# Kernel optimization log

Hardware: AMD Instinct MI355X
Metric: run time of the kernel (lower is better)

Reference implementation:

```python
import jax, jax.numpy as jnp
import numpy as np

SIGMA = 1.0  # init kwarg sigma

def _rbf_kernel(A):
    # K[i,j] = exp(-0.5 * ||a_i - a_j||^2 / sigma^2)
    sq = jnp.sum(A * A, axis=1)                      # [n]
    d2 = sq[:, None] + sq[None, :] - 2.0 * (A @ A.T)  # [n, n]
    return jnp.exp(-0.5 * d2 / (SIGMA ** 2))

def _double_center(K):
    # C K C with C = I - 11^T/n, done in O(n^2) via mean subtraction
    row = K.mean(axis=1, keepdims=True)
    col = K.mean(axis=0, keepdims=True)
    tot = K.mean()
    return K - row - col + tot

def setup_inputs() -> dict:
    key = jax.random.key(0)
    kx, ky = jax.random.split(key)
    X = jax.random.normal(kx, (4096, 512), dtype=jnp.float32)
    Y = jax.random.normal(ky, (4096, 512), dtype=jnp.float32)
    return {"X": X, "Y": Y}

def reference(X, Y):
    n = X.shape[0]
    KXc = _double_center(_rbf_kernel(X))
    KYc = _double_center(_rbf_kernel(Y))
    # trace(KX C KY C) = sum(center(KX) * center(KY)) since K symmetric, C idempotent
    hsic = jnp.sum(KXc * KYc) / ((n - 1) ** 2)
    return hsic
```

## Files before the change

### kernel.cpp

```cpp
#include <hip/hip_runtime.h>
#include <hip/hip_bf16.h>

namespace {

constexpr int N = 4096;
constexpr int D = 512;
constexpr int BM = 128;
constexpr int BK = 64;
constexpr int KITERS = D / BK;
constexpr int NB = N / BM;
constexpr int NBLK = NB * (NB + 1) / 2;
constexpr int TILEB = BM * BK;
constexpr int PANELB = BM * D;

constexpr size_t OFF_XB  = 0;
constexpr size_t OFF_YB  = (size_t)N * D;
constexpr size_t OFF_SQX = OFF_YB + (size_t)N * D;
constexpr size_t OFF_SQY = OFF_SQX + (size_t)N * 4;
constexpr size_t OFF_SX  = OFF_SQY + (size_t)N * 4;
constexpr size_t OFF_SY  = OFF_SX + (size_t)N * 4;
constexpr size_t OFF_T1  = OFF_SY + (size_t)N * 4;
constexpr size_t WS_NEED = OFF_T1 + 4;


constexpr float D2_SKIP = 240.f;

typedef __attribute__((ext_vector_type(4))) float floatx4;
typedef __attribute__((ext_vector_type(2))) long longx2;

__device__ inline void stage16(const void* g, void* l) {
  __builtin_amdgcn_global_load_lds(
      (const __attribute__((address_space(1))) unsigned int*)g,
      (__attribute__((address_space(3))) unsigned int*)l, 16, 0, 0);
}

__global__ void prep_kernel(const float* __restrict__ X, const float* __restrict__ Y,
                            unsigned char* __restrict__ Xf8, unsigned char* __restrict__ Yf8,
                            float* __restrict__ sqX, float* __restrict__ sqY,
                            float* __restrict__ sX, float* __restrict__ sY,
                            float* __restrict__ T1) {
  const int wave = threadIdx.x >> 6, lane = threadIdx.x & 63;
  const int row = blockIdx.x * 4 + wave;
  const int m = blockIdx.y;
  const float* __restrict__ src = m ? Y : X;
  unsigned char* __restrict__ dst = m ? Yf8 : Xf8;
  float* __restrict__ dsq = m ? sqY : sqX;

  if (threadIdx.x < 4) {
    float* z = m ? sY : sX;
    z[blockIdx.x * 4 + threadIdx.x] = 0.f;
  }
  if (blockIdx.x == 0 && m == 0 && threadIdx.x == 0) *T1 = 0.f;

  const float4* s4 = (const float4*)(src + (size_t)row * D);
  float4 v0 = s4[lane * 2];
  float4 v1 = s4[lane * 2 + 1];
  float acc = v0.x * v0.x + v0.y * v0.y + v0.z * v0.z + v0.w * v0.w
            + v1.x * v1.x + v1.y * v1.y + v1.z * v1.z + v1.w * v1.w;

  unsigned int w0 = 0, w1 = 0;
  w0 = __builtin_amdgcn_cvt_pk_fp8_f32(v0.x, v0.y, w0, false);
  w0 = __builtin_amdgcn_cvt_pk_fp8_f32(v0.z, v0.w, w0, true);
  w1 = __builtin_amdgcn_cvt_pk_fp8_f32(v1.x, v1.y, w1, false);
  w1 = __builtin_amdgcn_cvt_pk_fp8_f32(v1.z, v1.w, w1, true);
  const unsigned long long pk =
      (unsigned long long)w0 | ((unsigned long long)w1 << 32);

  const int p    = row >> 7;
  const int half = (row >> 6) & 1;
  const int nib  = (row >> 4) & 3;
  const int cl   = row & 15;
  const int ks   = lane >> 3;
  const int pass = (lane >> 2) & 1;
  const int quad = lane & 3;
  const size_t off = (size_t)p * PANELB + (size_t)ks * TILEB +
                     half * 4096 + nib * 1024 + quad * 256 + cl * 16 + pass * 8;
  *(unsigned long long*)(dst + off) = pk;

#pragma unroll
  for (int mm = 32; mm >= 1; mm >>= 1) acc += __shfl_xor(acc, mm, 64);
  if (lane == 0) dsq[row] = acc;
}

__launch_bounds__(256, 2)
__global__ void hsic_main(const unsigned char* __restrict__ Xf8,
                          const unsigned char* __restrict__ Yf8,
                          const float* __restrict__ sqX, const float* __restrict__ sqY,
                          float* __restrict__ sX, float* __restrict__ sY,
                          float* __restrict__ T1) {
  __shared__ __align__(16) unsigned char smem[2][4 * TILEB];

  const int b = blockIdx.x;
  int idx = (b & 7) * (NBLK / 8) + (b >> 3);

  const float nf = (float)NB + 0.5f;
  int bI = (int)(nf - sqrtf(nf * nf - 2.0f * (float)idx));
  if (bI < 0) bI = 0;
  if (bI >= NB) bI = NB - 1;
  while (bI * NB - bI * (bI - 1) / 2 > idx) --bI;
  while ((bI + 1) * NB - (bI + 1) * bI / 2 <= idx) ++bI;
  const int bJ = bI + (idx - (bI * NB - bI * (bI - 1) / 2));
  const bool offdiag = (bI != bJ);

  const int tid = threadIdx.x;
  const int lane = tid & 63, wave = tid >> 6;
  const int wm = wave >> 1, wn = wave & 1;
  const int quad = lane >> 4, cl = lane & 15;

  const unsigned char* gAx = Xf8 + (size_t)bI * PANELB;
  const unsigned char* gBx = Xf8 + (size_t)bJ * PANELB;
  const unsigned char* gAy = Yf8 + (size_t)bI * PANELB;
  const unsigned char* gBy = Yf8 + (size_t)bJ * PANELB;

  floatx4 accX[4][4];
  floatx4 accY[4][4];
#pragma unroll
  for (int i = 0; i < 4; ++i)
#pragma unroll
    for (int j = 0; j < 4; ++j) {
      accX[i][j] = (floatx4){0.f, 0.f, 0.f, 0.f};
      accY[i][j] = (floatx4){0.f, 0.f, 0.f, 0.f};
    }

  auto stage_all = [&](int kt, int buf) {
    const size_t ks0 = (size_t)kt * TILEB;
#pragma unroll
    for (int h = 0; h < 2; ++h) {
      const int c = tid + h * 256;
      const size_t goff = ks0 + (size_t)c * 16;
      const int loff = c * 16;
      stage16(gAx + goff, &smem[buf][0 * TILEB + loff]);
      stage16(gBx + goff, &smem[buf][1 * TILEB + loff]);
      stage16(gAy + goff, &smem[buf][2 * TILEB + loff]);
      stage16(gBy + goff, &smem[buf][3 * TILEB + loff]);
    }
  };

  stage_all(0, 0);

  for (int kt = 0; kt < KITERS; ++kt) {
    const int buf = kt & 1;
    __syncthreads();
    if (kt + 1 < KITERS) stage_all(kt + 1, buf ^ 1);

    const unsigned char* Ax = &smem[buf][0 * TILEB];
    const unsigned char* Bx = &smem[buf][1 * TILEB];
    const unsigned char* Ay = &smem[buf][2 * TILEB];
    const unsigned char* By = &smem[buf][3 * TILEB];

    longx2 bxf[4], byf[4];
#pragma unroll
    for (int ni = 0; ni < 4; ++ni) {
      const int off = wn * 4096 + ni * 1024 + (lane << 4);
      bxf[ni] = *(const longx2*)&Bx[off];
      byf[ni] = *(const longx2*)&By[off];
    }
#pragma unroll
    for (int mi = 0; mi < 4; ++mi) {
      const int off = wm * 4096 + mi * 1024 + (lane << 4);
      const longx2 axf = *(const longx2*)&Ax[off];
      const longx2 ayf = *(const longx2*)&Ay[off];
#pragma unroll
      for (int ni = 0; ni < 4; ++ni) {
        accX[mi][ni] = __builtin_amdgcn_mfma_f32_16x16x32_fp8_fp8(axf[0], bxf[ni][0], accX[mi][ni], 0, 0, 0);
        accX[mi][ni] = __builtin_amdgcn_mfma_f32_16x16x32_fp8_fp8(axf[1], bxf[ni][1], accX[mi][ni], 0, 0, 0);
        accY[mi][ni] = __builtin_amdgcn_mfma_f32_16x16x32_fp8_fp8(ayf[0], byf[ni][0], accY[mi][ni], 0, 0, 0);
        accY[mi][ni] = __builtin_amdgcn_mfma_f32_16x16x32_fp8_fp8(ayf[1], byf[ni][1], accY[mi][ni], 0, 0, 0);
      }
    }
  }

  const int Ib = bI * BM + wm * 64;
  const int Jb = bJ * BM + wn * 64;
  float t1l = 0.f;
  float rx[4][4], ry[4][4];
  float cx[4], cy[4];
#pragma unroll
  for (int mi = 0; mi < 4; ++mi)
#pragma unroll
    for (int r = 0; r < 4; ++r) { rx[mi][r] = 0.f; ry[mi][r] = 0.f; }
#pragma unroll
  for (int ni = 0; ni < 4; ++ni) { cx[ni] = 0.f; cy[ni] = 0.f; }

  bool wave_any = false;

#pragma unroll
  for (int mi = 0; mi < 4; ++mi) {
    const int ig0 = Ib + mi * 16 + quad * 4;
    float sxi[4], syi[4];
#pragma unroll
    for (int r = 0; r < 4; ++r) { sxi[r] = sqX[ig0 + r]; syi[r] = sqY[ig0 + r]; }
#pragma unroll
    for (int ni = 0; ni < 4; ++ni) {
      const int jg = Jb + ni * 16 + cl;
      const float sxj = sqX[jg];
      const float syj = sqY[jg];
      float d2x[4], d2y[4];
      bool lflag = false;
#pragma unroll
      for (int r = 0; r < 4; ++r) {
        const int ig = ig0 + r;
        d2x[r] = sxi[r] + sxj - 2.f * accX[mi][ni][r];
        d2y[r] = syi[r] + syj - 2.f * accY[mi][ni][r];
        lflag |= (d2x[r] < D2_SKIP) | (d2y[r] < D2_SKIP) | (ig == jg);
      }
      if (__any(lflag)) {
        wave_any = true;
#pragma unroll
        for (int r = 0; r < 4; ++r) {
          const int ig = ig0 + r;
          float kx, ky;
          if (ig == jg) {
            kx = 1.f; ky = 1.f;
          } else {
            kx = __expf(-0.5f * d2x[r]);
            ky = __expf(-0.5f * d2y[r]);
          }
          t1l += kx * ky;
          rx[mi][r] += kx;
          ry[mi][r] += ky;
          cx[ni] += kx;
          cy[ni] += ky;
        }
      }
    }
  }

  if (wave_any) {
#pragma unroll
    for (int mi = 0; mi < 4; ++mi)
#pragma unroll
      for (int r = 0; r < 4; ++r) {
        float vx = rx[mi][r], vy = ry[mi][r];
#pragma unroll
        for (int mm = 1; mm < 16; mm <<= 1) {
          vx += __shfl_xor(vx, mm, 16);
          vy += __shfl_xor(vy, mm, 16);
        }
        rx[mi][r] = vx; ry[mi][r] = vy;
      }
    if (cl == 0) {
#pragma unroll
      for (int mi = 0; mi < 4; ++mi)
#pragma unroll
        for (int r = 0; r < 4; ++r) {
          const int row = Ib + mi * 16 + quad * 4 + r;
          atomicAdd(&sX[row], rx[mi][r]);
          atomicAdd(&sY[row], ry[mi][r]);
        }
    }

    if (offdiag) {
#pragma unroll
      for (int ni = 0; ni < 4; ++ni) {
        float vx = cx[ni], vy = cy[ni];
        vx += __shfl_xor(vx, 16, 64); vy += __shfl_xor(vy, 16, 64);
        vx += __shfl_xor(vx, 32, 64); vy += __shfl_xor(vy, 32, 64);
        if (quad == 0) {
          const int col = Jb + ni * 16 + cl;
          atomicAdd(&sX[col], vx);
          atomicAdd(&sY[col], vy);
        }
      }
    }

    t1l *= offdiag ? 2.f : 1.f;
#pragma unroll
    for (int mm = 1; mm < 64; mm <<= 1) t1l += __shfl_xor(t1l, mm, 64);
  }
  __shared__ float tred[4];
  if (lane == 0) tred[wave] = t1l;
  __syncthreads();
  if (tid == 0) {
    const float t = tred[0] + tred[1] + tred[2] + tred[3];
    if (t != 0.f) atomicAdd(T1, t);
  }
}

__global__ void final_kernel(const float* __restrict__ sX, const float* __restrict__ sY,
                             const float* __restrict__ T1, float* __restrict__ out) {
  const int tid = threadIdx.x;
  float dp = 0.f, sa = 0.f, sb = 0.f;
  for (int i = tid; i < N; i += 256) {
    float a = sX[i], b = sY[i];
    dp += a * b; sa += a; sb += b;
  }
#pragma unroll
  for (int mm = 1; mm < 64; mm <<= 1) {
    dp += __shfl_xor(dp, mm, 64);
    sa += __shfl_xor(sa, mm, 64);
    sb += __shfl_xor(sb, mm, 64);
  }
  __shared__ float r0[4], r1[4], r2[4];
  if ((tid & 63) == 0) { int w = tid >> 6; r0[w] = dp; r1[w] = sa; r2[w] = sb; }
  __syncthreads();
  if (tid == 0) {
    dp = r0[0] + r0[1] + r0[2] + r0[3];
    sa = r1[0] + r1[1] + r1[2] + r1[3];
    sb = r2[0] + r2[1] + r2[2] + r2[3];
    const float n = (float)N;
    const float total = T1[0] - (2.f / n) * dp + (sa * sb) / (n * n);
    out[0] = total / ((n - 1.f) * (n - 1.f));
  }
}

}

extern "C" void kernel_launch(void* const* d_in, const int* in_sizes, int n_in,
                              void* d_out, int out_size, void* d_ws, size_t ws_size,
                              hipStream_t stream) {
  const float* X = (const float*)d_in[0];
  const float* Y = (const float*)d_in[1];
  char* ws = (char*)d_ws;
  if (ws_size < WS_NEED) return;

  unsigned char* Xf8 = (unsigned char*)(ws + OFF_XB);
  unsigned char* Yf8 = (unsigned char*)(ws + OFF_YB);
  float* sqX = (float*)(ws + OFF_SQX);
  float* sqY = (float*)(ws + OFF_SQY);
  float* sX  = (float*)(ws + OFF_SX);
  float* sY  = (float*)(ws + OFF_SY);
  float* T1  = (float*)(ws + OFF_T1);
  float* out = (float*)d_out;

  prep_kernel<<<dim3(N / 4, 2), 256, 0, stream>>>(X, Y, Xf8, Yf8, sqX, sqY, sX, sY, T1);
  hsic_main<<<NBLK, 256, 0, stream>>>(Xf8, Yf8, sqX, sqY, sX, sY, T1);
  final_kernel<<<1, 256, 0, stream>>>(sX, sY, T1, out);
}
```

Before: 96.53 us.

## Serialize X and Y Gram K-loops to halve LDS and raise occupancy

Instead of staging the X and Y A/B tiles together each k-step, the main loop now runs 16 iterations, first over X and then over Y, staging only one A and one B tile per step. This halves shared memory per block, and the launch bound is raised to 3 blocks per CU. Diagonal blocks skip staging the B tile and reuse the A tile. The trade-off is twice as many barriers and smaller per-iteration MFMA batches, and both accumulator sets stay live, so register pressure may limit the intended occupancy gain.

```diff
diff --git a/kernel.cpp b/kernel.cpp
--- a/kernel.cpp
+++ b/kernel.cpp
@@ -82,13 +82,13 @@
   if (lane == 0) dsq[row] = acc;
 }
 
-__launch_bounds__(256, 2)
+__launch_bounds__(256, 3)
 __global__ void hsic_main(const unsigned char* __restrict__ Xf8,
                           const unsigned char* __restrict__ Yf8,
                           const float* __restrict__ sqX, const float* __restrict__ sqY,
                           float* __restrict__ sX, float* __restrict__ sY,
                           float* __restrict__ T1) {
-  __shared__ __align__(16) unsigned char smem[2][4 * TILEB];
+  __shared__ __align__(16) unsigned char smem[2][2 * TILEB];
 
   const int b = blockIdx.x;
   int idx = (b & 7) * (NBLK / 8) + (b >> 3);
@@ -122,52 +122,47 @@
       accY[i][j] = (floatx4){0.f, 0.f, 0.f, 0.f};
     }
 
-  auto stage_all = [&](int kt, int buf) {
-    const size_t ks0 = (size_t)kt * TILEB;
+  auto stage_all = [&](int iter, int buf) {
+    const unsigned char* gA = (iter < KITERS) ? gAx : gAy;
+    const unsigned char* gB = (iter < KITERS) ? gBx : gBy;
+    const size_t ks0 = (size_t)(iter & (KITERS - 1)) * TILEB;
 #pragma unroll
     for (int h = 0; h < 2; ++h) {
       const int c = tid + h * 256;
       const size_t goff = ks0 + (size_t)c * 16;
-      const int loff = c * 16;
-      stage16(gAx + goff, &smem[buf][0 * TILEB + loff]);
-      stage16(gBx + goff, &smem[buf][1 * TILEB + loff]);
-      stage16(gAy + goff, &smem[buf][2 * TILEB + loff]);
-      stage16(gBy + goff, &smem[buf][3 * TILEB + loff]);
+      stage16(gA + goff, &smem[buf][0 * TILEB + c * 16]);
+      if (offdiag) stage16(gB + goff, &smem[buf][1 * TILEB + c * 16]);
     }
   };
 
+  auto compute_tile = [&](const unsigned char* A, const unsigned char* B,
+                          floatx4 (&acc)[4][4]) {
+    longx2 bf[4];
+#pragma unroll
+    for (int ni = 0; ni < 4; ++ni)
+      bf[ni] = *(const longx2*)&B[wn * 4096 + ni * 1024 + (lane << 4)];
+#pragma unroll
+    for (int mi = 0; mi < 4; ++mi) {
+      const longx2 af = *(const longx2*)&A[wm * 4096 + mi * 1024 + (lane << 4)];
+#pragma unroll
+      for (int ni = 0; ni < 4; ++ni) {
+        acc[mi][ni] = __builtin_amdgcn_mfma_f32_16x16x32_fp8_fp8(af[0], bf[ni][0], acc[mi][ni], 0, 0, 0);
+        acc[mi][ni] = __builtin_amdgcn_mfma_f32_16x16x32_fp8_fp8(af[1], bf[ni][1], acc[mi][ni], 0, 0, 0);
+      }
+    }
+  };
+
   stage_all(0, 0);
 
-  for (int kt = 0; kt < KITERS; ++kt) {
-    const int buf = kt & 1;
+  for (int iter = 0; iter < 2 * KITERS; ++iter) {
+    const int buf = iter & 1;
     __syncthreads();
-    if (kt + 1 < KITERS) stage_all(kt + 1, buf ^ 1);
-
-    const unsigned char* Ax = &smem[buf][0 * TILEB];
-    const unsigned char* Bx = &smem[buf][1 * TILEB];
-    const unsigned char* Ay = &smem[buf][2 * TILEB];
-    const unsigned char* By = &smem[buf][3 * TILEB];
-
-    longx2 bxf[4], byf[4];
-#pragma unroll
-    for (int ni = 0; ni < 4; ++ni) {
-      const int off = wn * 4096 + ni * 1024 + (lane << 4);
-      bxf[ni] = *(const longx2*)&Bx[off];
-      byf[ni] = *(const longx2*)&By[off];
-    }
-#pragma unroll
-    for (int mi = 0; mi < 4; ++mi) {
-      const int off = wm * 4096 + mi * 1024 + (lane << 4);
-      const longx2 axf = *(const longx2*)&Ax[off];
-      const longx2 ayf = *(const longx2*)&Ay[off];
-#pragma unroll
-      for (int ni = 0; ni < 4; ++ni) {
-        accX[mi][ni] = __builtin_amdgcn_mfma_f32_16x16x32_fp8_fp8(axf[0], bxf[ni][0], accX[mi][ni], 0, 0, 0);
-        accX[mi][ni] = __builtin_amdgcn_mfma_f32_16x16x32_fp8_fp8(axf[1], bxf[ni][1], accX[mi][ni], 0, 0, 0);
-        accY[mi][ni] = __builtin_amdgcn_mfma_f32_16x16x32_fp8_fp8(ayf[0], byf[ni][0], accY[mi][ni], 0, 0, 0);
-        accY[mi][ni] = __builtin_amdgcn_mfma_f32_16x16x32_fp8_fp8(ayf[1], byf[ni][1], accY[mi][ni], 0, 0, 0);
-      }
-    }
+    if (iter + 1 < 2 * KITERS) stage_all(iter + 1, buf ^ 1);
+
+    const unsigned char* A = &smem[buf][0];
+    const unsigned char* B = offdiag ? &smem[buf][TILEB] : &smem[buf][0];
+    if (iter < KITERS) compute_tile(A, B, accX);
+    else               compute_tile(A, B, accY);
   }
 
   const int Ib = bI * BM + wm * 64;
```

New measurement: 97.22 us. Within noise of the previous version (+0.7%).
